# Kernel optimization log

Measured on AMD Instinct MI355X. Metric: run time of the kernel, lower is better.

## Reference

```python
import jax, jax.numpy as jnp
import numpy as np

N_HEADS = 8
EPSILON = -50000.0


def setup_inputs() -> dict:
    key = jax.random.key(0)
    k1, k2, k3, k4, k5, k6 = jax.random.split(key, 6)
    B, S, D = 4, 2048, 512
    q_vec = jax.random.normal(k1, (B, S, D), dtype=jnp.float32)
    k_mat = jax.random.normal(k2, (B, S, D), dtype=jnp.float32)
    v_mat = jax.random.normal(k3, (B, S, D), dtype=jnp.float32)
    # mask: mostly valid keys with some padding masked out
    mask = jax.random.uniform(k4, (B, S)) < 0.9
    cutoff = jax.random.uniform(k5, (B, S), dtype=jnp.float32)
    W_out = jax.random.normal(k6, (D, D), dtype=jnp.float32) * (1.0 / np.sqrt(D))
    return {"q_vec": q_vec, "k_mat": k_mat, "v_mat": v_mat,
            "mask": mask, "cutoff": cutoff, "W_out": W_out}


def reference(q_vec, k_mat, v_mat, mask, cutoff, W_out):
    D = q_vec.shape[-1]
    H = N_HEADS
    dh = D // H
    # split heads: [B, S, D] -> [B, S, H, dh]
    q_ = q_vec.reshape(q_vec.shape[:-1] + (H, dh))
    k_ = k_mat.reshape(k_mat.shape[:-1] + (H, dh))
    v_ = v_mat.reshape(v_mat.shape[:-1] + (H, dh))
    # scores: [B, H, Sq, Sk]
    scores = jnp.einsum('bqhd,bkhd->bhqk', q_, k_) / jnp.sqrt(jnp.asarray(dh, q_vec.dtype))
    # additive mask over keys, then stable softmax
    scores = jnp.where(mask[:, None, None, :], scores, EPSILON)
    probs = jax.nn.softmax(scores, axis=-1)
    # post-softmax cutoff scaling per key
    probs = probs * cutoff[:, None, None, :]
    # attention output: [B, Sq, H, dh] -> [B, Sq, D]
    att = jnp.einsum('bhqk,bkhd->bqhd', probs, v_).reshape(q_vec.shape)
    return att @ W_out
```

## Files before the change

### kernel.cpp

```cpp
#include <hip/hip_runtime.h>
#include <hip/hip_bf16.h>
#include <stdint.h>

#define B_ 4
#define S_ 2048
#define D_ 512
#define H_ 8

typedef __attribute__((ext_vector_type(4))) float f32x4;
typedef __attribute__((ext_vector_type(16))) float f32x16;
typedef __attribute__((ext_vector_type(8))) short s16x8;

__device__ __forceinline__ unsigned short f2bf(float x) {
  union { float f; unsigned u; } v; v.f = x;
  unsigned r = v.u + 0x7FFFu + ((v.u >> 16) & 1u);
  return (unsigned short)(r >> 16);
}

__device__ __forceinline__ unsigned cvtpk_bf16(float lo, float hi) {
  unsigned r;
  asm("v_cvt_pk_bf16_f32 %0, %1, %2" : "=v"(r) : "v"(lo), "v"(hi));
  return r;
}

__device__ __forceinline__ void plswap(unsigned &a, unsigned &b) {
  asm("v_permlane32_swap_b32 %0, %1" : "+v"(a), "+v"(b));
}

__device__ __forceinline__ void gload16(const void* g, void* lds) {
  __builtin_amdgcn_global_load_lds(
      (const __attribute__((address_space(1))) void*)g,
      (__attribute__((address_space(3))) void*)lds, 16, 0, 0);
}

__global__ __launch_bounds__(256) void conv_kv_kernel(
    const float* __restrict__ km, const float* __restrict__ vm,
    const float* __restrict__ cut, const int* __restrict__ mask,
    unsigned short* __restrict__ Kbf, unsigned short* __restrict__ Vt,
    unsigned short* __restrict__ fmg)
{
  const int st = blockIdx.x, bh = blockIdx.y;
  const int b = bh >> 3, h = bh & 7;
  const int s0 = st * 64;
  __shared__ unsigned short sT[64][68];
  const int tid = threadIdx.x;
#pragma unroll
  for (int j = 0; j < 4; ++j) {
    const int li = tid + j * 256;
    const int r  = li >> 4;
    const int c4 = (li & 15) * 4;
    const size_t g = ((size_t)(b * S_ + s0 + r)) * D_ + h * 64 + c4;
    const float4 kv = *(const float4*)(km + g);
    const float4 vv = *(const float4*)(vm + g);
    const int mk = mask[(size_t)b * S_ + s0 + r];
    const float f = mk ? cut[(size_t)b * S_ + s0 + r] : 0.f;
    *(ushort4*)(Kbf + ((size_t)(bh * S_ + s0 + r)) * 64 + c4) =
        make_ushort4(f2bf(kv.x), f2bf(kv.y), f2bf(kv.z), f2bf(kv.w));
    sT[r][c4 + 0] = f2bf(vv.x * f);
    sT[r][c4 + 1] = f2bf(vv.y * f);
    sT[r][c4 + 2] = f2bf(vv.z * f);
    sT[r][c4 + 3] = f2bf(vv.w * f);
    if (h == 0 && c4 == 0)
      fmg[(size_t)b * S_ + s0 + r] = mk ? (unsigned short)0x3F80 : (unsigned short)0;
  }
  __syncthreads();
#pragma unroll
  for (int j = 0; j < 4; ++j) {
    const int li = tid + j * 256;
    const int dh = li >> 4;
    const int s4 = (li & 15) * 4;
    *(ushort4*)(Vt + ((size_t)(bh * 64 + dh)) * S_ + s0 + s4) =
        make_ushort4(sT[s4 + 0][dh], sT[s4 + 1][dh], sT[s4 + 2][dh], sT[s4 + 3][dh]);
  }
}

__global__ __launch_bounds__(256) void conv_w_kernel(
    const float* __restrict__ W, unsigned short* __restrict__ Wt)
{
  const int k0 = blockIdx.x * 64, n0 = blockIdx.y * 64;
  __shared__ unsigned short sT[64][68];
  const int tid = threadIdx.x;
#pragma unroll
  for (int j = 0; j < 4; ++j) {
    const int li = tid + j * 256;
    const int r  = li >> 4;
    const int c4 = (li & 15) * 4;
    const float4 wv = *(const float4*)(W + (size_t)(k0 + r) * 512 + n0 + c4);
    sT[r][c4 + 0] = f2bf(wv.x);
    sT[r][c4 + 1] = f2bf(wv.y);
    sT[r][c4 + 2] = f2bf(wv.z);
    sT[r][c4 + 3] = f2bf(wv.w);
  }
  __syncthreads();
#pragma unroll
  for (int j = 0; j < 4; ++j) {
    const int li = tid + j * 256;
    const int n  = li >> 4;
    const int k4 = (li & 15) * 4;
    *(ushort4*)(Wt + (size_t)(n0 + n) * 512 + k0 + k4) =
        make_ushort4(sT[k4 + 0][n], sT[k4 + 1][n], sT[k4 + 2][n], sT[k4 + 3][n]);
  }
}

__global__ __launch_bounds__(256) void attn_mfma_kernel(
    const float* __restrict__ qv, const unsigned short* __restrict__ Kbf,
    const unsigned short* __restrict__ Vt, const unsigned short* __restrict__ fmg,
    unsigned short* __restrict__ attb)
{
  __shared__ unsigned short sK[2][64 * 64];
  __shared__ unsigned short sV[2][64 * 64];
  __shared__ unsigned short sF[2][64];

  const int qt = blockIdx.x, bh = blockIdx.y;
  const int b = bh >> 3, h = bh & 7;
  const int tid = threadIdx.x, w = tid >> 6, l = tid & 63;
  const int l31 = l & 31, hi = l >> 5;
  const int q0 = qt * 128 + w * 32;

  s16x8 qf[4];
  {
    const float* qp = qv + ((size_t)(b * S_ + q0 + l31)) * D_ + h * 64 + hi * 8;
#pragma unroll
    for (int kc = 0; kc < 4; ++kc) {
      const float4 a0 = *(const float4*)(qp + kc * 16);
      const float4 a1 = *(const float4*)(qp + kc * 16 + 4);
      union { unsigned u[4]; s16x8 v; } t;
      t.u[0] = cvtpk_bf16(a0.x * 0.125f, a0.y * 0.125f);
      t.u[1] = cvtpk_bf16(a0.z * 0.125f, a0.w * 0.125f);
      t.u[2] = cvtpk_bf16(a1.x * 0.125f, a1.y * 0.125f);
      t.u[3] = cvtpk_bf16(a1.z * 0.125f, a1.w * 0.125f);
      qf[kc] = t.v;
    }
  }

  f32x16 o0, o1, lacc;
#pragma unroll
  for (int r = 0; r < 16; ++r) { o0[r] = 0.f; o1[r] = 0.f; lacc[r] = 0.f; }

  const int swl = ((l & 7) ^ (l >> 3)) * 16;
  const int r8  = l >> 3;

  auto STAGE = [&](int bufi, int kt) {
    const int k0 = kt * 64;
#pragma unroll
    for (int c = 0; c < 2; ++c) {
      const int chunk = w * 2 + c;
      const int r = chunk * 8 + r8;
      gload16((const char*)(Kbf + ((size_t)bh * S_ + k0 + r) * 64) + swl,
              (char*)sK[bufi] + chunk * 1024);
      gload16((const char*)(Vt + ((size_t)(bh * 64 + r)) * S_ + k0) + swl,
              (char*)sV[bufi] + chunk * 1024);
    }
    if (tid < 8)
      gload16((const char*)(fmg + (size_t)b * S_ + k0) + tid * 16, (char*)sF[bufi]);
  };

  STAGE(0, 0);
  __syncthreads();

  int buf = 0;
  for (int kt = 0; kt < S_ / 64; ++kt) {
    if (kt + 1 < S_ / 64) STAGE(buf ^ 1, kt + 1);

    const char* pK = (const char*)sK[buf];
    const char* pV = (const char*)sV[buf];
    const char* pF = (const char*)sF[buf];

    f32x16 sacc0, sacc1;
#pragma unroll
    for (int r = 0; r < 16; ++r) { sacc0[r] = 0.f; sacc1[r] = 0.f; }
    __builtin_amdgcn_s_setprio(1);
#pragma unroll
    for (int kc = 0; kc < 4; ++kc) {
      const int cb = kc * 32 + hi * 16;
      const int row0 = l31, row1 = 32 + l31;
      const s16x8 kf0 = *(const s16x8*)(pK + row0 * 128 + (cb ^ ((row0 & 7) << 4)));
      const s16x8 kf1 = *(const s16x8*)(pK + row1 * 128 + (cb ^ ((row1 & 7) << 4)));
      sacc0 = __builtin_amdgcn_mfma_f32_32x32x16_bf16(kf0, qf[kc], sacc0, 0, 0, 0);
      sacc1 = __builtin_amdgcn_mfma_f32_32x32x16_bf16(kf1, qf[kc], sacc1, 0, 0, 0);
    }
    __builtin_amdgcn_s_setprio(0);

    float p0[16], p1[16];
#pragma unroll
    for (int r = 0; r < 16; ++r) { p0[r] = __expf(sacc0[r]); p1[r] = __expf(sacc1[r]); }

    __builtin_amdgcn_s_setprio(1);
#pragma unroll
    for (int ks2 = 0; ks2 < 4; ++ks2) {
      const float* ps = (ks2 < 2) ? p0 : p1;
      const int rb = (ks2 & 1) * 8;
      unsigned a0 = cvtpk_bf16(ps[rb + 0], ps[rb + 1]);
      unsigned a1 = cvtpk_bf16(ps[rb + 2], ps[rb + 3]);
      unsigned b0 = cvtpk_bf16(ps[rb + 4], ps[rb + 5]);
      unsigned b1 = cvtpk_bf16(ps[rb + 6], ps[rb + 7]);
      plswap(a0, b0);
      plswap(a1, b1);
      union { unsigned u[4]; s16x8 v; } pa;
      pa.u[0] = a0; pa.u[1] = a1; pa.u[2] = b0; pa.u[3] = b1;

      const int cb = ks2 * 32 + hi * 16;
      const int rv0 = l31, rv1 = 32 + l31;
      const s16x8 vb0 = *(const s16x8*)(pV + rv0 * 128 + (cb ^ ((rv0 & 7) << 4)));
      const s16x8 vb1 = *(const s16x8*)(pV + rv1 * 128 + (cb ^ ((rv1 & 7) << 4)));
      const s16x8 fmf = *(const s16x8*)(pF + cb);
      o0   = __builtin_amdgcn_mfma_f32_32x32x16_bf16(pa.v, vb0, o0, 0, 0, 0);
      o1   = __builtin_amdgcn_mfma_f32_32x32x16_bf16(pa.v, vb1, o1, 0, 0, 0);
      lacc = __builtin_amdgcn_mfma_f32_32x32x16_bf16(pa.v, fmf, lacc, 0, 0, 0);
    }
    __builtin_amdgcn_s_setprio(0);

    __syncthreads();
    buf ^= 1;
  }

  unsigned short* ob = attb + ((size_t)(b * S_)) * D_ + h * 64;
#pragma unroll
  for (int r = 0; r < 16; ++r) {
    const float inv = 1.f / lacc[r];
    const int q = q0 + (r & 3) + 8 * (r >> 2) + 4 * hi;
    ob[(size_t)q * D_ + l31]      = f2bf(o0[r] * inv);
    ob[(size_t)q * D_ + 32 + l31] = f2bf(o1[r] * inv);
  }
}

__global__ __launch_bounds__(256) void proj_mfma_kernel(
    const unsigned short* __restrict__ A, const unsigned short* __restrict__ Wt,
    float* __restrict__ out)
{
  __shared__ unsigned short sA[128 * 64];
  __shared__ unsigned short sB[128 * 64];
  const int m0 = blockIdx.x * 128, n0 = blockIdx.y * 128;
  const int tid = threadIdx.x, w = tid >> 6, l = tid & 63;
  const int l15 = l & 15, l4 = l >> 4;
  const int wm = (w >> 1) * 64, wn = (w & 1) * 64;
  const int swl = ((l & 7) ^ (l >> 3)) * 16;
  const int r8 = l >> 3;

  f32x4 acc[4][4];
#pragma unroll
  for (int i = 0; i < 4; ++i)
#pragma unroll
    for (int j = 0; j < 4; ++j) acc[i][j] = (f32x4){0.f, 0.f, 0.f, 0.f};

  for (int kt = 0; kt < 8; ++kt) {
    const int k0 = kt * 64;
    __syncthreads();
#pragma unroll
    for (int c = 0; c < 4; ++c) {
      const int chunk = w * 4 + c;
      const int r = chunk * 8 + r8;
      gload16((const char*)(A + ((size_t)(m0 + r)) * 512 + k0) + swl,
              (char*)sA + chunk * 1024);
      gload16((const char*)(Wt + ((size_t)(n0 + r)) * 512 + k0) + swl,
              (char*)sB + chunk * 1024);
    }
    __syncthreads();
#pragma unroll
    for (int ks = 0; ks < 2; ++ks) {
      s16x8 af[4], bf_[4];
#pragma unroll
      for (int mb = 0; mb < 4; ++mb) {
        const int row = wm + mb * 16 + l15;
        const int sz = (row & 7) << 4;
        af[mb] = *(const s16x8*)((const char*)sA + row * 128 + ((ks * 64 + l4 * 16) ^ sz));
      }
#pragma unroll
      for (int nb = 0; nb < 4; ++nb) {
        const int row = wn + nb * 16 + l15;
        const int sz = (row & 7) << 4;
        bf_[nb] = *(const s16x8*)((const char*)sB + row * 128 + ((ks * 64 + l4 * 16) ^ sz));
      }
#pragma unroll
      for (int mb = 0; mb < 4; ++mb)
#pragma unroll
        for (int nb = 0; nb < 4; ++nb)
          acc[mb][nb] = __builtin_amdgcn_mfma_f32_16x16x32_bf16(af[mb], bf_[nb], acc[mb][nb], 0, 0, 0);
    }
  }
#pragma unroll
  for (int mb = 0; mb < 4; ++mb)
#pragma unroll
    for (int nb = 0; nb < 4; ++nb)
#pragma unroll
      for (int r = 0; r < 4; ++r)
        out[(size_t)(m0 + wm + mb * 16 + l4 * 4 + r) * 512 + n0 + wn + nb * 16 + l15] =
            acc[mb][nb][r];
}

extern "C" void kernel_launch(void* const* d_in, const int* in_sizes, int n_in,
                              void* d_out, int out_size, void* d_ws, size_t ws_size,
                              hipStream_t stream) {
  const float* q    = (const float*)d_in[0];
  const float* k    = (const float*)d_in[1];
  const float* v    = (const float*)d_in[2];
  const int*   mask = (const int*)d_in[3];
  const float* cut  = (const float*)d_in[4];
  const float* W    = (const float*)d_in[5];
  float* out = (float*)d_out;

  char* ws = (char*)d_ws;
  unsigned short* Kbf  = (unsigned short*)(ws);
  unsigned short* Vt   = (unsigned short*)(ws + (8u << 20));
  unsigned short* attb = (unsigned short*)(ws + (16u << 20));
  unsigned short* Wt   = (unsigned short*)(ws + (24u << 20));
  unsigned short* fmg  = (unsigned short*)(ws + (25u << 20));

  conv_kv_kernel<<<dim3(S_ / 64, B_ * H_), 256, 0, stream>>>(k, v, cut, mask, Kbf, Vt, fmg);
  conv_w_kernel<<<dim3(8, 8), 256, 0, stream>>>(W, Wt);
  attn_mfma_kernel<<<dim3(S_ / 128, B_ * H_), 256, 0, stream>>>(q, Kbf, Vt, fmg, attb);
  proj_mfma_kernel<<<dim3(64, 4), 256, 0, stream>>>(attb, Wt, out);
}
```

Baseline: 81.92 us.

## Split attention key range across wave pairs and reduce partials in shared memory

Each block's four waves now split into two query halves and two key halves. Each wave handles 64 queries (two 32-row subtiles) over half the keys, so every loaded K fragment serves two MFMAs and V fragments are reused across two query subtiles. The partial outputs and denominators are then combined through LDS at the end. The mask/cutoff vector is read straight from global memory into registers instead of being staged in LDS. The intent is better operand reuse per LDS read and more MFMA work per wave. The cost is higher register pressure (six accumulators plus P fragments) and an extra shared-memory reduction pass, with the launch bound now requesting 2 blocks per CU.

Result: faster. 79.62 us (-2.8%).

```diff
diff --git a/kernel.cpp b/kernel.cpp
--- a/kernel.cpp
+++ b/kernel.cpp
@@ -102,24 +102,26 @@
   }
 }
 
-__global__ __launch_bounds__(256) void attn_mfma_kernel(
+__global__ __launch_bounds__(256, 2) void attn_mfma_kernel(
     const float* __restrict__ qv, const unsigned short* __restrict__ Kbf,
     const unsigned short* __restrict__ Vt, const unsigned short* __restrict__ fmg,
     unsigned short* __restrict__ attb)
 {
-  __shared__ unsigned short sK[2][64 * 64];
-  __shared__ unsigned short sV[2][64 * 64];
-  __shared__ unsigned short sF[2][64];
+  __shared__ unsigned short sK[2][2][4096];
+  __shared__ unsigned short sV[2][2][4096];
 
   const int qt = blockIdx.x, bh = blockIdx.y;
   const int b = bh >> 3, h = bh & 7;
   const int tid = threadIdx.x, w = tid >> 6, l = tid & 63;
   const int l31 = l & 31, hi = l >> 5;
-  const int q0 = qt * 128 + w * 32;
-
-  s16x8 qf[4];
-  {
-    const float* qp = qv + ((size_t)(b * S_ + q0 + l31)) * D_ + h * 64 + hi * 8;
+  const int qh = w & 1, kh = w >> 1;
+  const int kbase = kh * 1024;
+
+  s16x8 qf[2][4];
+#pragma unroll
+  for (int s = 0; s < 2; ++s) {
+    const int qrow = qt * 128 + qh * 64 + s * 32 + l31;
+    const float* qp = qv + ((size_t)(b * S_ + qrow)) * D_ + h * 64 + hi * 8;
 #pragma unroll
     for (int kc = 0; kc < 4; ++kc) {
       const float4 a0 = *(const float4*)(qp + kc * 16);
@@ -129,84 +131,107 @@
       t.u[1] = cvtpk_bf16(a0.z * 0.125f, a0.w * 0.125f);
       t.u[2] = cvtpk_bf16(a1.x * 0.125f, a1.y * 0.125f);
       t.u[3] = cvtpk_bf16(a1.z * 0.125f, a1.w * 0.125f);
-      qf[kc] = t.v;
-    }
-  }
-
-  f32x16 o0, o1, lacc;
-#pragma unroll
-  for (int r = 0; r < 16; ++r) { o0[r] = 0.f; o1[r] = 0.f; lacc[r] = 0.f; }
+      qf[s][kc] = t.v;
+    }
+  }
+
+  f32x16 o00, o01, o10, o11, la0, la1;
+#pragma unroll
+  for (int r = 0; r < 16; ++r) {
+    o00[r] = 0.f; o01[r] = 0.f; o10[r] = 0.f; o11[r] = 0.f;
+    la0[r] = 0.f; la1[r] = 0.f;
+  }
 
   const int swl = ((l & 7) ^ (l >> 3)) * 16;
   const int r8  = l >> 3;
+  const char* KbfB = (const char*)(Kbf + (size_t)bh * S_ * 64);
+  const char* VtB  = (const char*)(Vt + (size_t)bh * 64 * S_);
 
   auto STAGE = [&](int bufi, int kt) {
-    const int k0 = kt * 64;
-#pragma unroll
-    for (int c = 0; c < 2; ++c) {
-      const int chunk = w * 2 + c;
-      const int r = chunk * 8 + r8;
-      gload16((const char*)(Kbf + ((size_t)bh * S_ + k0 + r) * 64) + swl,
-              (char*)sK[bufi] + chunk * 1024);
-      gload16((const char*)(Vt + ((size_t)(bh * 64 + r)) * S_ + k0) + swl,
-              (char*)sV[bufi] + chunk * 1024);
-    }
-    if (tid < 8)
-      gload16((const char*)(fmg + (size_t)b * S_ + k0) + tid * 16, (char*)sF[bufi]);
+    const int k0 = kbase + kt * 64;
+#pragma unroll
+    for (int c = 0; c < 4; ++c) {
+      const int chunk = qh * 4 + c;
+      const int row = chunk * 8 + r8;
+      gload16(KbfB + (size_t)(k0 + row) * 128 + swl, (char*)sK[kh][bufi] + chunk * 1024);
+      gload16(VtB + ((size_t)row * S_ + k0) * 2 + swl, (char*)sV[kh][bufi] + chunk * 1024);
+    }
   };
 
   STAGE(0, 0);
   __syncthreads();
 
   int buf = 0;
-  for (int kt = 0; kt < S_ / 64; ++kt) {
-    if (kt + 1 < S_ / 64) STAGE(buf ^ 1, kt + 1);
-
-    const char* pK = (const char*)sK[buf];
-    const char* pV = (const char*)sV[buf];
-    const char* pF = (const char*)sF[buf];
-
-    f32x16 sacc0, sacc1;
-#pragma unroll
-    for (int r = 0; r < 16; ++r) { sacc0[r] = 0.f; sacc1[r] = 0.f; }
+  for (int kt = 0; kt < 16; ++kt) {
+    const int k0 = kbase + kt * 64;
+    s16x8 fmf[4];
+#pragma unroll
+    for (int ks = 0; ks < 4; ++ks)
+      fmf[ks] = *(const s16x8*)(fmg + (size_t)b * S_ + k0 + ks * 16 + hi * 8);
+
+    if (kt + 1 < 16) STAGE(buf ^ 1, kt + 1);
+
+    const char* pK = (const char*)sK[kh][buf];
+    const char* pV = (const char*)sV[kh][buf];
+
+    s16x8 pa[2][4];
+#pragma unroll
+    for (int k2 = 0; k2 < 2; ++k2) {
+      f32x16 sa0, sa1;
+#pragma unroll
+      for (int r = 0; r < 16; ++r) { sa0[r] = 0.f; sa1[r] = 0.f; }
+      __builtin_amdgcn_s_setprio(1);
+#pragma unroll
+      for (int kc = 0; kc < 4; ++kc) {
+        const int row = k2 * 32 + l31;
+        const s16x8 kf = *(const s16x8*)(pK + row * 128 +
+                          ((kc * 32 + hi * 16) ^ ((row & 7) << 4)));
+        sa0 = __builtin_amdgcn_mfma_f32_32x32x16_bf16(kf, qf[0][kc], sa0, 0, 0, 0);
+        sa1 = __builtin_amdgcn_mfma_f32_32x32x16_bf16(kf, qf[1][kc], sa1, 0, 0, 0);
+      }
+      __builtin_amdgcn_s_setprio(0);
+      float p0[16], p1[16];
+#pragma unroll
+      for (int r = 0; r < 16; ++r) { p0[r] = __expf(sa0[r]); p1[r] = __expf(sa1[r]); }
+#pragma unroll
+      for (int ks = 0; ks < 2; ++ks) {
+        const int rb = ks * 8;
+        {
+          unsigned a0 = cvtpk_bf16(p0[rb + 0], p0[rb + 1]);
+          unsigned a1 = cvtpk_bf16(p0[rb + 2], p0[rb + 3]);
+          unsigned b0 = cvtpk_bf16(p0[rb + 4], p0[rb + 5]);
+          unsigned b1 = cvtpk_bf16(p0[rb + 6], p0[rb + 7]);
+          plswap(a0, b0); plswap(a1, b1);
+          union { unsigned u[4]; s16x8 v; } t;
+          t.u[0] = a0; t.u[1] = a1; t.u[2] = b0; t.u[3] = b1;
+          pa[0][k2 * 2 + ks] = t.v;
+        }
+        {
+          unsigned a0 = cvtpk_bf16(p1[rb + 0], p1[rb + 1]);
+          unsigned a1 = cvtpk_bf16(p1[rb + 2], p1[rb + 3]);
+          unsigned b0 = cvtpk_bf16(p1[rb + 4], p1[rb + 5]);
+          unsigned b1 = cvtpk_bf16(p1[rb + 6], p1[rb + 7]);
+          plswap(a0, b0); plswap(a1, b1);
+          union { unsigned u[4]; s16x8 v; } t;
+          t.u[0] = a0; t.u[1] = a1; t.u[2] = b0; t.u[3] = b1;
+          pa[1][k2 * 2 + ks] = t.v;
+        }
+      }
+    }
+
     __builtin_amdgcn_s_setprio(1);
 #pragma unroll
-    for (int kc = 0; kc < 4; ++kc) {
-      const int cb = kc * 32 + hi * 16;
-      const int row0 = l31, row1 = 32 + l31;
-      const s16x8 kf0 = *(const s16x8*)(pK + row0 * 128 + (cb ^ ((row0 & 7) << 4)));
-      const s16x8 kf1 = *(const s16x8*)(pK + row1 * 128 + (cb ^ ((row1 & 7) << 4)));
-      sacc0 = __builtin_amdgcn_mfma_f32_32x32x16_bf16(kf0, qf[kc], sacc0, 0, 0, 0);
-      sacc1 = __builtin_amdgcn_mfma_f32_32x32x16_bf16(kf1, qf[kc], sacc1, 0, 0, 0);
-    }
-    __builtin_amdgcn_s_setprio(0);
-
-    float p0[16], p1[16];
-#pragma unroll
-    for (int r = 0; r < 16; ++r) { p0[r] = __expf(sacc0[r]); p1[r] = __expf(sacc1[r]); }
-
-    __builtin_amdgcn_s_setprio(1);
-#pragma unroll
     for (int ks2 = 0; ks2 < 4; ++ks2) {
-      const float* ps = (ks2 < 2) ? p0 : p1;
-      const int rb = (ks2 & 1) * 8;
-      unsigned a0 = cvtpk_bf16(ps[rb + 0], ps[rb + 1]);
-      unsigned a1 = cvtpk_bf16(ps[rb + 2], ps[rb + 3]);
-      unsigned b0 = cvtpk_bf16(ps[rb + 4], ps[rb + 5]);
-      unsigned b1 = cvtpk_bf16(ps[rb + 6], ps[rb + 7]);
-      plswap(a0, b0);
-      plswap(a1, b1);
-      union { unsigned u[4]; s16x8 v; } pa;
-      pa.u[0] = a0; pa.u[1] = a1; pa.u[2] = b0; pa.u[3] = b1;
-
       const int cb = ks2 * 32 + hi * 16;
       const int rv0 = l31, rv1 = 32 + l31;
       const s16x8 vb0 = *(const s16x8*)(pV + rv0 * 128 + (cb ^ ((rv0 & 7) << 4)));
       const s16x8 vb1 = *(const s16x8*)(pV + rv1 * 128 + (cb ^ ((rv1 & 7) << 4)));
-      const s16x8 fmf = *(const s16x8*)(pF + cb);
-      o0   = __builtin_amdgcn_mfma_f32_32x32x16_bf16(pa.v, vb0, o0, 0, 0, 0);
-      o1   = __builtin_amdgcn_mfma_f32_32x32x16_bf16(pa.v, vb1, o1, 0, 0, 0);
-      lacc = __builtin_amdgcn_mfma_f32_32x32x16_bf16(pa.v, fmf, lacc, 0, 0, 0);
+      o00 = __builtin_amdgcn_mfma_f32_32x32x16_bf16(pa[0][ks2], vb0, o00, 0, 0, 0);
+      o01 = __builtin_amdgcn_mfma_f32_32x32x16_bf16(pa[0][ks2], vb1, o01, 0, 0, 0);
+      o10 = __builtin_amdgcn_mfma_f32_32x32x16_bf16(pa[1][ks2], vb0, o10, 0, 0, 0);
+      o11 = __builtin_amdgcn_mfma_f32_32x32x16_bf16(pa[1][ks2], vb1, o11, 0, 0, 0);
+      la0 = __builtin_amdgcn_mfma_f32_32x32x16_bf16(pa[0][ks2], fmf[ks2], la0, 0, 0, 0);
+      la1 = __builtin_amdgcn_mfma_f32_32x32x16_bf16(pa[1][ks2], fmf[ks2], la1, 0, 0, 0);
     }
     __builtin_amdgcn_s_setprio(0);
 
@@ -214,13 +239,56 @@
     buf ^= 1;
   }
 
-  unsigned short* ob = attb + ((size_t)(b * S_)) * D_ + h * 64;
+  float* po = (float*)&sK[0][0][0];
+  float* pl = (float*)&sV[0][0][0];
+
+  if (kh == 0) {
+#pragma unroll
+    for (int half = 0; half < 2; ++half)
+#pragma unroll
+      for (int r = 0; r < 16; ++r) {
+        po[(((qh * 2 + 0) * 2 + half) * 16 + r) * 64 + l] = (half == 0) ? o00[r] : o01[r];
+        po[(((qh * 2 + 1) * 2 + half) * 16 + r) * 64 + l] = (half == 0) ? o10[r] : o11[r];
+      }
+    if (l31 == 0) {
+#pragma unroll
+      for (int r = 0; r < 16; ++r) {
+        pl[((qh * 2 + 0) * 2 + hi) * 16 + r] = la0[r];
+        pl[((qh * 2 + 1) * 2 + hi) * 16 + r] = la1[r];
+      }
+    }
+  }
+  __syncthreads();
+  if (kh == 1) {
+#pragma unroll
+    for (int half = 0; half < 2; ++half)
+#pragma unroll
+      for (int r = 0; r < 16; ++r) {
+        po[(((qh * 2 + 0) * 2 + half) * 16 + r) * 64 + l] += (half == 0) ? o00[r] : o01[r];
+        po[(((qh * 2 + 1) * 2 + half) * 16 + r) * 64 + l] += (half == 0) ? o10[r] : o11[r];
+      }
+    if (l31 == 0) {
+#pragma unroll
+      for (int r = 0; r < 16; ++r) {
+        pl[((qh * 2 + 0) * 2 + hi) * 16 + r] += la0[r];
+        pl[((qh * 2 + 1) * 2 + hi) * 16 + r] += la1[r];
+      }
+    }
+  }
+  __syncthreads();
+
+  const int qm = w & 1, sm = w >> 1;
+  unsigned short* ob = attb + ((size_t)b * S_) * D_ + h * 64;
 #pragma unroll
   for (int r = 0; r < 16; ++r) {
-    const float inv = 1.f / lacc[r];
-    const int q = q0 + (r & 3) + 8 * (r >> 2) + 4 * hi;
-    ob[(size_t)q * D_ + l31]      = f2bf(o0[r] * inv);
-    ob[(size_t)q * D_ + 32 + l31] = f2bf(o1[r] * inv);
+    const float ls = pl[((qm * 2 + sm) * 2 + hi) * 16 + r];
+    const float inv = 1.f / ls;
+    const int q = qt * 128 + qm * 64 + sm * 32 + (r & 3) + 8 * (r >> 2) + 4 * hi;
+#pragma unroll
+    for (int half = 0; half < 2; ++half) {
+      const float ov = po[(((qm * 2 + sm) * 2 + half) * 16 + r) * 64 + l];
+      ob[(size_t)q * D_ + half * 32 + l31] = f2bf(ov * inv);
+    }
   }
 }
 
```
